# Kernel optimization log

Measured on AMD Instinct MI355X. Metric: run time of the kernel, lower is better.

The kernel has to match this reference:

```python
import jax, jax.numpy as jnp
import numpy as np

GROUPS = 32
EPS = 1e-5
HEADS = 8
HEAD_DIM = 40
INNER = HEADS * HEAD_DIM  # 320
QUERY_DIM = 320
CONTEXT_DIM = 768


def setup_inputs() -> dict:
    key = jax.random.key(0)
    ks = jax.random.split(key, 9)
    B, C, H, W = 16, QUERY_DIM, 64, 64
    Lc = 77
    x = jax.random.normal(ks[0], (B, C, H, W), dtype=jnp.float32)
    context = jax.random.normal(ks[1], (B, Lc, CONTEXT_DIM), dtype=jnp.float32)
    # Linear weights in torch layout (out_features, in_features), no bias for q/k/v
    Wq = jax.random.normal(ks[2], (INNER, QUERY_DIM), dtype=jnp.float32) * (QUERY_DIM ** -0.5)
    Wk = jax.random.normal(ks[3], (INNER, CONTEXT_DIM), dtype=jnp.float32) * (CONTEXT_DIM ** -0.5)
    Wv = jax.random.normal(ks[4], (INNER, CONTEXT_DIM), dtype=jnp.float32) * (CONTEXT_DIM ** -0.5)
    Wo = jax.random.normal(ks[5], (QUERY_DIM, INNER), dtype=jnp.float32) * (INNER ** -0.5)
    bo = jnp.zeros((QUERY_DIM,), dtype=jnp.float32)
    gn_scale = jnp.ones((QUERY_DIM,), dtype=jnp.float32)
    gn_bias = jnp.zeros((QUERY_DIM,), dtype=jnp.float32)
    return {"x": x, "context": context, "Wq": Wq, "Wk": Wk, "Wv": Wv,
            "Wo": Wo, "bo": bo, "gn_scale": gn_scale, "gn_bias": gn_bias}


def _group_norm(x, scale, bias):
    # x: [B, C, H, W]
    B, C, H, W = x.shape
    xg = x.reshape(B, GROUPS, C // GROUPS, H, W)
    mean = jnp.mean(xg, axis=(2, 3, 4), keepdims=True)
    var = jnp.var(xg, axis=(2, 3, 4), keepdims=True)
    xn = ((xg - mean) * jax.lax.rsqrt(var + EPS)).reshape(B, C, H, W)
    return xn * scale[None, :, None, None] + bias[None, :, None, None]


def reference(x, context, Wq, Wk, Wv, Wo, bo, gn_scale, gn_bias):
    B, C, H, W = x.shape
    residual = x
    xn = _group_norm(x, gn_scale, gn_bias)
    # (B, C, H, W) -> (B, H*W, C)
    tokens = xn.reshape(B, C, H * W).transpose(0, 2, 1)
    S = H * W
    Lc = context.shape[1]
    scale = HEAD_DIM ** -0.5
    # projections (Linear: x @ W.T); split heads -> [B, h, S, d]
    q = jnp.einsum('bsc,ec->bse', tokens, Wq).reshape(B, S, HEADS, HEAD_DIM).transpose(0, 2, 1, 3)
    k = jnp.einsum('blc,ec->ble', context, Wk).reshape(B, Lc, HEADS, HEAD_DIM).transpose(0, 2, 1, 3)
    v = jnp.einsum('blc,ec->ble', context, Wv).reshape(B, Lc, HEADS, HEAD_DIM).transpose(0, 2, 1, 3)
    scores = jnp.einsum('bhsd,bhkd->bhsk', q, k) * scale  # [B, h, S, Lc]
    attn = jax.nn.softmax(scores, axis=-1)
    out = jnp.einsum('bhsk,bhkd->bhsd', attn, v)  # [B, h, S, d]
    out = out.transpose(0, 2, 1, 3).reshape(B, S, INNER)
    out = jnp.einsum('bse,ce->bsc', out, Wo) + bo  # to_out (dropout is identity at eval)
    out = out.transpose(0, 2, 1).reshape(B, C, H, W)
    return out + residual
```

## Files before the change

### kernel.cpp

```cpp
#include <hip/hip_runtime.h>
#include <hip/hip_bf16.h>
#include <stdint.h>

#define B_    16
#define C_    320
#define S_    4096
#define G_    32
#define LC    77
#define CTX   768
#define HEADS 8
#define HD    40

typedef __bf16 bf16x8_t __attribute__((ext_vector_type(8)));
typedef float  f32x4_t  __attribute__((ext_vector_type(4)));

__device__ __forceinline__ unsigned short f2bf(float f) {
    union { float f; unsigned int u; } v; v.f = f;
    unsigned int r = v.u + 0x7fffu + ((v.u >> 16) & 1u);
    return (unsigned short)(r >> 16);
}
__device__ __forceinline__ float bf2f(unsigned short h) {
    union { unsigned int u; float f; } v; v.u = ((unsigned int)h) << 16;
    return v.f;
}

__device__ __forceinline__ void gload16(const void* g, void* l) {
    __builtin_amdgcn_global_load_lds(
        (const __attribute__((address_space(1))) unsigned int*)g,
        (__attribute__((address_space(3))) unsigned int*)l, 16, 0, 0);
}

__global__ __launch_bounds__(256) void gn_stats(const float* __restrict__ x,
                                                float2* __restrict__ mr) {
    int bg = blockIdx.x;
    const float4* p = (const float4*)(x + (size_t)bg * 40960);
    float s = 0.f, s2 = 0.f;
    for (int i = threadIdx.x; i < 10240; i += 256) {
        float4 v = p[i];
        s  += v.x + v.y + v.z + v.w;
        s2 += v.x * v.x + v.y * v.y + v.z * v.z + v.w * v.w;
    }
    for (int o = 32; o; o >>= 1) {
        s  += __shfl_down(s, o);
        s2 += __shfl_down(s2, o);
    }
    __shared__ float2 red[4];
    int lane = threadIdx.x & 63, wid = threadIdx.x >> 6;
    if (lane == 0) red[wid] = make_float2(s, s2);
    __syncthreads();
    if (threadIdx.x == 0) {
        float a = 0.f, c = 0.f;
        for (int i = 0; i < 4; i++) { a += red[i].x; c += red[i].y; }
        float mean = a / 40960.f;
        float var  = c / 40960.f - mean * mean;
        mr[bg] = make_float2(mean, rsqrtf(var + 1e-5f));
    }
}

__global__ __launch_bounds__(256) void castw(const float* __restrict__ s,
                                             unsigned short* __restrict__ d) {
    int i = blockIdx.x * 256 + threadIdx.x;
    float4 v = ((const float4*)s)[i];
    ushort4 o;
    o.x = f2bf(v.x); o.y = f2bf(v.y); o.z = f2bf(v.z); o.w = f2bf(v.w);
    ((ushort4*)d)[i] = o;
}

__global__ __launch_bounds__(256) void norm_tr(const float* __restrict__ x,
                                               const float2* __restrict__ mr,
                                               const float* __restrict__ gns,
                                               const float* __restrict__ gnb,
                                               unsigned short* __restrict__ tok) {
    int s0 = blockIdx.x * 32, c0 = blockIdx.y * 32, b = blockIdx.z;
    __shared__ unsigned short t[32][33];
    int tx = threadIdx.x & 31, ty = threadIdx.x >> 5;
    #pragma unroll
    for (int i = 0; i < 4; i++) {
        int cl = i * 8 + ty;
        int c = c0 + cl;
        float2 m = mr[b * 32 + c / 10];
        float v = x[((size_t)(b * 320 + c)) * 4096 + s0 + tx];
        v = (v - m.x) * m.y * gns[c] + gnb[c];
        t[cl][tx] = f2bf(v);
    }
    __syncthreads();
    #pragma unroll
    for (int i = 0; i < 4; i++) {
        int sl = i * 8 + ty;
        tok[((size_t)b * 4096 + s0 + sl) * 320 + c0 + tx] = t[tx][sl];
    }
}

__global__ __launch_bounds__(256) void ukern(const float* __restrict__ Wk,
                                             const float* __restrict__ Wq,
                                             unsigned short* __restrict__ Ut) {
    int c = blockIdx.x, h = blockIdx.y;
    int t = threadIdx.x;
    float a0 = 0.f, a1 = 0.f, a2 = 0.f;
    for (int d = 0; d < HD; d++) {
        float wq = Wq[(size_t)(h * HD + d) * 320 + c];
        const float* wkr = Wk + (size_t)(h * HD + d) * CTX;
        a0 += wq * wkr[t];
        a1 += wq * wkr[t + 256];
        a2 += wq * wkr[t + 512];
    }
    unsigned short* o = Ut + ((size_t)h * 320 + c) * CTX;
    o[t]       = f2bf(a0);
    o[t + 256] = f2bf(a1);
    o[t + 512] = f2bf(a2);
}

__global__ __launch_bounds__(256) void kvM_gemm(const float* __restrict__ ctx,
                                                const float* __restrict__ Wv,
                                                const unsigned short* __restrict__ Ut,
                                                unsigned short* __restrict__ vout,
                                                unsigned short* __restrict__ Mout) {
    __shared__ unsigned short la[64][32], lb[64][32];
    int bm = blockIdx.x, bn = blockIdx.y;
    int tid = threadIdx.x, lane = tid & 63, wid = tid >> 6;
    int wm = wid >> 1, wn = wid & 1;
    int lr = tid >> 2, lc = (tid & 3) * 8;
    int fr = lane & 15, kk = (lane >> 4) * 8;

    int arow = bm * 64 + lr; if (arow > 1231) arow = 1231;
    const float* ap = ctx + (size_t)arow * CTX;
    bool isV = (bn < 5);
    const float* wp = isV ? (Wv + (size_t)(bn * 64 + lr) * CTX) : nullptr;
    const unsigned short* up = isV ? nullptr
        : (Ut + ((size_t)((bn - 5) / 5) * 320 + (size_t)((bn - 5) % 5) * 64 + lr) * CTX);

    f32x4_t acc[2][2] = {};
    for (int k0 = 0; k0 < CTX; k0 += 32) {
        float4 a4 = *(const float4*)&ap[k0 + lc];
        float4 a5 = *(const float4*)&ap[k0 + lc + 4];
        ushort4 pa0 = { f2bf(a4.x), f2bf(a4.y), f2bf(a4.z), f2bf(a4.w) };
        ushort4 pa1 = { f2bf(a5.x), f2bf(a5.y), f2bf(a5.z), f2bf(a5.w) };
        *(ushort4*)&la[lr][lc]     = pa0;
        *(ushort4*)&la[lr][lc + 4] = pa1;
        if (isV) {
            float4 w4 = *(const float4*)&wp[k0 + lc];
            float4 w5 = *(const float4*)&wp[k0 + lc + 4];
            ushort4 pw0 = { f2bf(w4.x), f2bf(w4.y), f2bf(w4.z), f2bf(w4.w) };
            ushort4 pw1 = { f2bf(w5.x), f2bf(w5.y), f2bf(w5.z), f2bf(w5.w) };
            *(ushort4*)&lb[lr][lc]     = pw0;
            *(ushort4*)&lb[lr][lc + 4] = pw1;
        } else {
            *(uint4*)&lb[lr][lc] = *(const uint4*)&up[k0 + lc];
        }
        __syncthreads();
        bf16x8_t a0 = *(const bf16x8_t*)&la[wm * 32 + fr][kk];
        bf16x8_t a1 = *(const bf16x8_t*)&la[wm * 32 + 16 + fr][kk];
        bf16x8_t b0 = *(const bf16x8_t*)&lb[wn * 32 + fr][kk];
        bf16x8_t b1 = *(const bf16x8_t*)&lb[wn * 32 + 16 + fr][kk];
        acc[0][0] = __builtin_amdgcn_mfma_f32_16x16x32_bf16(a0, b0, acc[0][0], 0, 0, 0);
        acc[0][1] = __builtin_amdgcn_mfma_f32_16x16x32_bf16(a0, b1, acc[0][1], 0, 0, 0);
        acc[1][0] = __builtin_amdgcn_mfma_f32_16x16x32_bf16(a1, b0, acc[1][0], 0, 0, 0);
        acc[1][1] = __builtin_amdgcn_mfma_f32_16x16x32_bf16(a1, b1, acc[1][1], 0, 0, 0);
        __syncthreads();
    }
    int rg = (lane >> 4) * 4;
    #pragma unroll
    for (int mf = 0; mf < 2; mf++)
        #pragma unroll
        for (int nf = 0; nf < 2; nf++)
            #pragma unroll
            for (int r = 0; r < 4; r++) {
                int row = bm * 64 + wm * 32 + mf * 16 + rg + r;
                if (row < 1232) {
                    int coloff = wn * 32 + nf * 16 + fr;
                    unsigned short val = f2bf(acc[mf][nf][r]);
                    if (isV) {
                        vout[(size_t)row * 320 + bn * 64 + coloff] = val;
                    } else {
                        int bb = row / 77, kv = row - bb * 77;
                        int hh = (bn - 5) / 5;
                        int c = ((bn - 5) % 5) * 64 + coloff;
                        size_t tile = ((size_t)bb * 8 + hh) * 25600;
                        int idx16 = kv * 40 + (c >> 3);
                        int swz = idx16 ^ (kv & 7);
                        Mout[tile + (size_t)swz * 8 + (c & 7)] = val;
                    }
                }
            }
}

__global__ __launch_bounds__(256, 2) void attn4(const unsigned short* __restrict__ tok,
                                                const unsigned short* __restrict__ M,
                                                const unsigned short* __restrict__ v,
                                                unsigned short* __restrict__ att) {
    __shared__ unsigned short Msr[25600];
    __shared__ unsigned short Vt[48][104];
    unsigned short (*Ps)[104] = (unsigned short (*)[104])Msr;

    int tid = threadIdx.x;
    int qt = blockIdx.x, b = blockIdx.y;
    int q0 = qt * 128;
    int lane = tid & 63, wv = tid >> 6;
    int fr = lane & 15, fg = lane >> 4;
    const float scale = 0.15811388300841898f;

    {
        uint4 z = {0, 0, 0, 0};
        uint4* p = (uint4*)&Vt[0][0];
        for (int i = tid; i < 624; i += 256) p[i] = z;
    }

    {
        const unsigned short* Mt = M + ((size_t)b * 8 + 0) * 25600;
        #pragma unroll
        for (int i = 0; i < 13; i++) {
            int u = i * 256 + tid;
            if (u < 3200) gload16(Mt + (size_t)u * 8, &Msr[u * 8]);
        }
    }

    uint4 vreg0, vreg1;
    {
        int r = tid / 5, sg = tid % 5;
        vreg0 = *(const uint4*)&v[((size_t)(b * LC + r)) * 320 + sg * 8];
        int idx = tid + 256;
        if (idx < 385) {
            r = idx / 5; sg = idx % 5;
            vreg1 = *(const uint4*)&v[((size_t)(b * LC + r)) * 320 + sg * 8];
        }
    }

    bf16x8_t atok[2][10];
    const size_t tokbase = ((size_t)b * S_ + q0) * 320;
    #pragma unroll
    for (int mf = 0; mf < 2; mf++)
        #pragma unroll
        for (int k = 0; k < 10; k++)
            atok[mf][k] = *(const bf16x8_t*)&tok[tokbase + (size_t)(wv * 32 + mf * 16 + fr) * 320 + k * 32 + fg * 8];

    __syncthreads();

    for (int h = 0; h < 8; h++) {
        {
            unsigned short e[8];
            int r = tid / 5, sg = tid % 5;
            *(uint4*)e = vreg0;
            #pragma unroll
            for (int j = 0; j < 8; j++) Vt[sg * 8 + j][r] = e[j];
            int idx = tid + 256;
            if (idx < 385) {
                r = idx / 5; sg = idx % 5;
                *(uint4*)e = vreg1;
                #pragma unroll
                for (int j = 0; j < 8; j++) Vt[sg * 8 + j][r] = e[j];
            }
        }
        if (h < 7) {
            int r = tid / 5, sg = tid % 5;
            vreg0 = *(const uint4*)&v[((size_t)(b * LC + r)) * 320 + (h + 1) * HD + sg * 8];
            int idx = tid + 256;
            if (idx < 385) {
                r = idx / 5; sg = idx % 5;
                vreg1 = *(const uint4*)&v[((size_t)(b * LC + r)) * 320 + (h + 1) * HD + sg * 8];
            }
        }

        f32x4_t sc[2][5] = {};
        #pragma unroll
        for (int k = 0; k < 10; k++) {
            bf16x8_t bb[5];
            #pragma unroll
            for (int nf = 0; nf < 5; nf++) {
                int idx16 = (nf * 16 + fr) * 40 + k * 4 + fg;
                bb[nf] = *(const bf16x8_t*)&Msr[(size_t)(idx16 ^ (fr & 7)) * 8];
            }
            #pragma unroll
            for (int mf = 0; mf < 2; mf++)
                #pragma unroll
                for (int nf = 0; nf < 5; nf++)
                    sc[mf][nf] = __builtin_amdgcn_mfma_f32_16x16x32_bf16(atok[mf][k], bb[nf], sc[mf][nf], 0, 0, 0);
        }
        __syncthreads();

        {
            uint4 z = {0, 0, 0, 0};
            int zr = wv * 32 + (lane >> 1);
            *(uint4*)((char*)&Ps[zr][80] + (lane & 1) * 16) = z;
        }

        float mx[2][4], sm[2][4];
        #pragma unroll
        for (int mf = 0; mf < 2; mf++)
            #pragma unroll
            for (int r = 0; r < 4; r++) {
                float m = -1e30f;
                #pragma unroll
                for (int nf = 0; nf < 5; nf++) {
                    float s = sc[mf][nf][r] * scale;
                    if (nf * 16 + fr >= LC) s = -1e30f;
                    sc[mf][nf][r] = s;
                    m = fmaxf(m, s);
                }
                mx[mf][r] = m;
            }
        #pragma unroll
        for (int off = 1; off < 16; off <<= 1)
            #pragma unroll
            for (int mf = 0; mf < 2; mf++)
                #pragma unroll
                for (int r = 0; r < 4; r++)
                    mx[mf][r] = fmaxf(mx[mf][r], __shfl_xor(mx[mf][r], off));
        #pragma unroll
        for (int mf = 0; mf < 2; mf++)
            #pragma unroll
            for (int r = 0; r < 4; r++) {
                float s = 0.f;
                #pragma unroll
                for (int nf = 0; nf < 5; nf++) {
                    float p = __expf(sc[mf][nf][r] - mx[mf][r]);
                    sc[mf][nf][r] = p;
                    s += p;
                }
                sm[mf][r] = s;
            }
        #pragma unroll
        for (int off = 1; off < 16; off <<= 1)
            #pragma unroll
            for (int mf = 0; mf < 2; mf++)
                #pragma unroll
                for (int r = 0; r < 4; r++)
                    sm[mf][r] += __shfl_xor(sm[mf][r], off);

        #pragma unroll
        for (int mf = 0; mf < 2; mf++)
            #pragma unroll
            for (int nf = 0; nf < 5; nf++)
                #pragma unroll
                for (int r = 0; r < 4; r++)
                    Ps[wv * 32 + mf * 16 + fg * 4 + r][nf * 16 + fr] = f2bf(sc[mf][nf][r]);

        f32x4_t ov[2][3] = {};
        #pragma unroll
        for (int ks = 0; ks < 3; ks++) {
            bf16x8_t vb[3];
            #pragma unroll
            for (int nf = 0; nf < 3; nf++)
                vb[nf] = *(const bf16x8_t*)&Vt[nf * 16 + fr][ks * 32 + fg * 8];
            #pragma unroll
            for (int mf = 0; mf < 2; mf++) {
                bf16x8_t pa = *(const bf16x8_t*)&Ps[wv * 32 + mf * 16 + fr][ks * 32 + fg * 8];
                #pragma unroll
                for (int nf = 0; nf < 3; nf++)
                    ov[mf][nf] = __builtin_amdgcn_mfma_f32_16x16x32_bf16(pa, vb[nf], ov[mf][nf], 0, 0, 0);
            }
        }
        __syncthreads();

        if (h < 7) {
            const unsigned short* Mn = M + ((size_t)b * 8 + h + 1) * 25600;
            #pragma unroll
            for (int i = 0; i < 13; i++) {
                int u = i * 256 + tid;
                if (u < 3200) gload16(Mn + (size_t)u * 8, &Msr[u * 8]);
            }
        }

        #pragma unroll
        for (int mf = 0; mf < 2; mf++) {
            float inv[4];
            #pragma unroll
            for (int r = 0; r < 4; r++) inv[r] = 1.f / sm[mf][r];
            #pragma unroll
            for (int nf = 0; nf < 3; nf++) {
                int d = nf * 16 + fr;
                if (d < HD) {
                    #pragma unroll
                    for (int r = 0; r < 4; r++) {
                        int qrow = q0 + wv * 32 + mf * 16 + fg * 4 + r;
                        att[((size_t)(b * S_ + qrow)) * 320 + h * HD + d] = f2bf(ov[mf][nf][r] * inv[r]);
                    }
                }
            }
        }
        __syncthreads();
    }
}

__device__ __forceinline__ void gemm_core(const unsigned short* __restrict__ Ab,
                                          const unsigned short* __restrict__ Wb,
                                          unsigned short la[64][32],
                                          unsigned short lb[64][32],
                                          f32x4_t acc[2][2]) {
    int tid = threadIdx.x, lane = tid & 63, wid = tid >> 6;
    int wm = wid >> 1, wn = wid & 1;
    int lr = tid >> 2, lc = (tid & 3) * 8;
    int fr = lane & 15, kk = (lane >> 4) * 8;
    for (int k0 = 0; k0 < 320; k0 += 32) {
        *(uint4*)&la[lr][lc] = *(const uint4*)&Ab[(size_t)lr * 320 + k0 + lc];
        *(uint4*)&lb[lr][lc] = *(const uint4*)&Wb[(size_t)lr * 320 + k0 + lc];
        __syncthreads();
        bf16x8_t a0 = *(const bf16x8_t*)&la[wm * 32 + fr][kk];
        bf16x8_t a1 = *(const bf16x8_t*)&la[wm * 32 + 16 + fr][kk];
        bf16x8_t b0 = *(const bf16x8_t*)&lb[wn * 32 + fr][kk];
        bf16x8_t b1 = *(const bf16x8_t*)&lb[wn * 32 + 16 + fr][kk];
        acc[0][0] = __builtin_amdgcn_mfma_f32_16x16x32_bf16(a0, b0, acc[0][0], 0, 0, 0);
        acc[0][1] = __builtin_amdgcn_mfma_f32_16x16x32_bf16(a0, b1, acc[0][1], 0, 0, 0);
        acc[1][0] = __builtin_amdgcn_mfma_f32_16x16x32_bf16(a1, b0, acc[1][0], 0, 0, 0);
        acc[1][1] = __builtin_amdgcn_mfma_f32_16x16x32_bf16(a1, b1, acc[1][1], 0, 0, 0);
        __syncthreads();
    }
}

__global__ __launch_bounds__(256) void gemm_oproj(const unsigned short* __restrict__ A,
                                                  const unsigned short* __restrict__ W,
                                                  const float* __restrict__ bo,
                                                  const float* __restrict__ resid,
                                                  float* __restrict__ out) {
    __shared__ unsigned short la[64][32], lb[64][32];
    __shared__ float lt[64][65];
    int bm = blockIdx.x, bn = blockIdx.y, b = blockIdx.z;
    const unsigned short* Ab = A + ((size_t)b * S_ + bm * 64) * 320;
    const unsigned short* Wb = W + (size_t)bn * 64 * 320;
    f32x4_t acc[2][2] = {};
    gemm_core(Ab, Wb, la, lb, acc);
    int tid = threadIdx.x, lane = tid & 63, wid = tid >> 6;
    int wm = wid >> 1, wn = wid & 1;
    int fr = lane & 15, rg = (lane >> 4) * 4;
    #pragma unroll
    for (int mf = 0; mf < 2; mf++)
        #pragma unroll
        for (int nf = 0; nf < 2; nf++)
            #pragma unroll
            for (int r = 0; r < 4; r++)
                lt[wm * 32 + mf * 16 + rg + r][wn * 32 + nf * 16 + fr] = acc[mf][nf][r];
    __syncthreads();
    #pragma unroll
    for (int p = 0; p < 16; p++) {
        int nl = p * 4 + (tid >> 6);
        int sl = tid & 63;
        int n = bn * 64 + nl, s = bm * 64 + sl;
        size_t idx = ((size_t)b * 320 + n) * 4096 + s;
        out[idx] = lt[sl][nl] + bo[n] + resid[idx];
    }
}

extern "C" void kernel_launch(void* const* d_in, const int* in_sizes, int n_in,
                              void* d_out, int out_size, void* d_ws, size_t ws_size,
                              hipStream_t stream) {
    const float* x    = (const float*)d_in[0];
    const float* ctx  = (const float*)d_in[1];
    const float* Wq   = (const float*)d_in[2];
    const float* Wk   = (const float*)d_in[3];
    const float* Wv   = (const float*)d_in[4];
    const float* Wo   = (const float*)d_in[5];
    const float* bo   = (const float*)d_in[6];
    const float* gns  = (const float*)d_in[7];
    const float* gnb  = (const float*)d_in[8];
    float* out = (float*)d_out;

    char* ws = (char*)d_ws;
    float2*         mr    = (float2*)(ws + 0);
    unsigned short* wo_bf = (unsigned short*)(ws + 4096);
    unsigned short* v_bf  = (unsigned short*)(ws + 208896);
    unsigned short* Mbuf  = (unsigned short*)(ws + 997376);
    unsigned short* tok   = (unsigned short*)(ws + 7550976);
    unsigned short* att   = (unsigned short*)(ws + 49494016);
    unsigned short* Ut    = att;

    gn_stats<<<512, 256, 0, stream>>>(x, mr);
    castw<<<100, 256, 0, stream>>>(Wo, wo_bf);
    ukern<<<dim3(320, 8), 256, 0, stream>>>(Wk, Wq, Ut);
    kvM_gemm<<<dim3(20, 45), 256, 0, stream>>>(ctx, Wv, Ut, v_bf, Mbuf);
    norm_tr<<<dim3(128, 10, 16), 256, 0, stream>>>(x, mr, gns, gnb, tok);
    attn4<<<dim3(32, 16), 256, 0, stream>>>(tok, Mbuf, v_bf, att);
    gemm_oproj<<<dim3(64, 5, 16), 256, 0, stream>>>(att, wo_bf, bo, x, out);
}
```

Measured before the change: 209.9 us.

## Compute full 320-wide output tile per block in out-projection GEMM

The output-projection GEMM now gives each block a 64-token tile across all 320 output channels. Each wave computes 80 channels as a transposed product (W·A^T), so accumulator registers map straight to the channel-major output layout. This removes the LDS transpose staging buffer and the five-fold re-read of the attention activations across N-blocks. Tiles are loaded through gload16 (async global-to-LDS) into padded 40-wide rows. The larger accumulator array (20 fragments) raises register pressure, and the grid shrinks to 1024 blocks.

```diff
diff --git a/kernel.cpp b/kernel.cpp
--- a/kernel.cpp
+++ b/kernel.cpp
@@ -381,61 +381,71 @@
     }
 }
 
-__device__ __forceinline__ void gemm_core(const unsigned short* __restrict__ Ab,
-                                          const unsigned short* __restrict__ Wb,
-                                          unsigned short la[64][32],
-                                          unsigned short lb[64][32],
-                                          f32x4_t acc[2][2]) {
-    int tid = threadIdx.x, lane = tid & 63, wid = tid >> 6;
-    int wm = wid >> 1, wn = wid & 1;
-    int lr = tid >> 2, lc = (tid & 3) * 8;
-    int fr = lane & 15, kk = (lane >> 4) * 8;
+__global__ __launch_bounds__(256) void gemm_oproj2(const unsigned short* __restrict__ att,
+                                                   const unsigned short* __restrict__ wo,
+                                                   const float* __restrict__ bo,
+                                                   const float* __restrict__ resid,
+                                                   float* __restrict__ out) {
+    __shared__ unsigned short lw[320 * 40];
+    __shared__ unsigned short la[64 * 40];
+    int tid = threadIdx.x, lane = tid & 63, wv = tid >> 6;
+    int fr = lane & 15, fg = lane >> 4;
+    int bm = blockIdx.x, b = blockIdx.y;
+    int s0 = bm * 64;
+    const size_t abase = ((size_t)b * S_ + s0) * 320;
+
+    f32x4_t acc[5][4] = {};
+
     for (int k0 = 0; k0 < 320; k0 += 32) {
-        *(uint4*)&la[lr][lc] = *(const uint4*)&Ab[(size_t)lr * 320 + k0 + lc];
-        *(uint4*)&lb[lr][lc] = *(const uint4*)&Wb[(size_t)lr * 320 + k0 + lc];
-        __syncthreads();
-        bf16x8_t a0 = *(const bf16x8_t*)&la[wm * 32 + fr][kk];
-        bf16x8_t a1 = *(const bf16x8_t*)&la[wm * 32 + 16 + fr][kk];
-        bf16x8_t b0 = *(const bf16x8_t*)&lb[wn * 32 + fr][kk];
-        bf16x8_t b1 = *(const bf16x8_t*)&lb[wn * 32 + 16 + fr][kk];
-        acc[0][0] = __builtin_amdgcn_mfma_f32_16x16x32_bf16(a0, b0, acc[0][0], 0, 0, 0);
-        acc[0][1] = __builtin_amdgcn_mfma_f32_16x16x32_bf16(a0, b1, acc[0][1], 0, 0, 0);
-        acc[1][0] = __builtin_amdgcn_mfma_f32_16x16x32_bf16(a1, b0, acc[1][0], 0, 0, 0);
-        acc[1][1] = __builtin_amdgcn_mfma_f32_16x16x32_bf16(a1, b1, acc[1][1], 0, 0, 0);
-        __syncthreads();
-    }
-}
-
-__global__ __launch_bounds__(256) void gemm_oproj(const unsigned short* __restrict__ A,
-                                                  const unsigned short* __restrict__ W,
-                                                  const float* __restrict__ bo,
-                                                  const float* __restrict__ resid,
-                                                  float* __restrict__ out) {
-    __shared__ unsigned short la[64][32], lb[64][32];
-    __shared__ float lt[64][65];
-    int bm = blockIdx.x, bn = blockIdx.y, b = blockIdx.z;
-    const unsigned short* Ab = A + ((size_t)b * S_ + bm * 64) * 320;
-    const unsigned short* Wb = W + (size_t)bn * 64 * 320;
-    f32x4_t acc[2][2] = {};
-    gemm_core(Ab, Wb, la, lb, acc);
-    int tid = threadIdx.x, lane = tid & 63, wid = tid >> 6;
-    int wm = wid >> 1, wn = wid & 1;
-    int fr = lane & 15, rg = (lane >> 4) * 4;
+        #pragma unroll
+        for (int i = 0; i < 7; i++) {
+            int u = i * 256 + tid;
+            if (u < 1600) {
+                int row = u / 5, ch = u % 5;
+                int c = ch < 4 ? ch : 0;
+                gload16(wo + (size_t)row * 320 + k0 + c * 8, &lw[(size_t)u * 8]);
+            }
+        }
+        {
+            int u = tid;
+            int row = u / 5, ch = u % 5;
+            int c = ch < 4 ? ch : 0;
+            gload16(att + abase + (size_t)row * 320 + k0 + c * 8, &la[(size_t)u * 8]);
+            u = tid + 256;
+            if (u < 320) {
+                row = u / 5; ch = u % 5; c = ch < 4 ? ch : 0;
+                gload16(att + abase + (size_t)row * 320 + k0 + c * 8, &la[(size_t)u * 8]);
+            }
+        }
+        __syncthreads();
+        bf16x8_t bfrag[4];
+        #pragma unroll
+        for (int sf = 0; sf < 4; sf++)
+            bfrag[sf] = *(const bf16x8_t*)&la[(sf * 16 + fr) * 40 + fg * 8];
+        #pragma unroll
+        for (int nf = 0; nf < 5; nf++) {
+            bf16x8_t afrag = *(const bf16x8_t*)&lw[(wv * 80 + nf * 16 + fr) * 40 + fg * 8];
+            #pragma unroll
+            for (int sf = 0; sf < 4; sf++)
+                acc[nf][sf] = __builtin_amdgcn_mfma_f32_16x16x32_bf16(afrag, bfrag[sf], acc[nf][sf], 0, 0, 0);
+        }
+        __syncthreads();
+    }
+
+    int nbase = wv * 80;
     #pragma unroll
-    for (int mf = 0; mf < 2; mf++)
-        #pragma unroll
-        for (int nf = 0; nf < 2; nf++)
-            #pragma unroll
-            for (int r = 0; r < 4; r++)
-                lt[wm * 32 + mf * 16 + rg + r][wn * 32 + nf * 16 + fr] = acc[mf][nf][r];
-    __syncthreads();
-    #pragma unroll
-    for (int p = 0; p < 16; p++) {
-        int nl = p * 4 + (tid >> 6);
-        int sl = tid & 63;
-        int n = bn * 64 + nl, s = bm * 64 + sl;
-        size_t idx = ((size_t)b * 320 + n) * 4096 + s;
-        out[idx] = lt[sl][nl] + bo[n] + resid[idx];
+    for (int nf = 0; nf < 5; nf++) {
+        #pragma unroll
+        for (int r = 0; r < 4; r++) {
+            int n = nbase + nf * 16 + fg * 4 + r;
+            float bov = bo[n];
+            size_t rowb = ((size_t)(b * 320 + n)) * 4096 + s0;
+            #pragma unroll
+            for (int sf = 0; sf < 4; sf++) {
+                int s = sf * 16 + fr;
+                out[rowb + s] = acc[nf][sf][r] + bov + resid[rowb + s];
+            }
+        }
     }
 }
 
@@ -468,5 +478,5 @@
     kvM_gemm<<<dim3(20, 45), 256, 0, stream>>>(ctx, Wv, Ut, v_bf, Mbuf);
     norm_tr<<<dim3(128, 10, 16), 256, 0, stream>>>(x, mr, gns, gnb, tok);
     attn4<<<dim3(32, 16), 256, 0, stream>>>(tok, Mbuf, v_bf, att);
-    gemm_oproj<<<dim3(64, 5, 16), 256, 0, stream>>>(att, wo_bf, bo, x, out);
-}
+    gemm_oproj2<<<dim3(64, 16), 256, 0, stream>>>(att, wo_bf, bo, x, out);
+}
```

Result: faster. 184.1 us (-12.3%).
